# Optimization experiments

Measured on AMD Instinct MI355X. Metric: run time of the kernel, lower is better.

The kernel has to match this reference:

```python
import jax, jax.numpy as jnp
import numpy as np


def setup_inputs() -> dict:
    key = jax.random.key(0)
    k1, k2 = jax.random.split(key)
    num_experts, input_size, output_size = 8, 512, 512
    expert_size = 32768  # tokens per expert (equal load; total = 262144)
    total_tokens = num_experts * expert_size
    inputs = jax.random.normal(k1, (total_tokens, input_size), dtype=jnp.float32)
    # experts stored [num_experts, output_size, input_size], matching F.linear convention
    weight = jax.random.normal(k2, (num_experts, output_size, input_size), dtype=jnp.float32) * (1.0 / np.sqrt(input_size))
    return {"inputs": inputs, "weight": weight, "expert_size": expert_size}


def reference(inputs, weight, expert_size):
    # inputs: [T, in] sorted by expert, equal expert_size per expert.
    # Equivalent of: split by expert_size, F.linear(x_i, weight[i]), concat.
    num_experts = weight.shape[0]
    x = inputs.reshape(num_experts, expert_size, inputs.shape[-1])  # [E, t, in]
    out = jnp.einsum("eti,eoi->eto", x, weight)  # grouped GEMM, [E, t, out]
    return out.reshape(num_experts * expert_size, weight.shape[1])
```

## Files before the change

### kernel.cpp

```cpp
#include <hip/hip_runtime.h>
#include <hip/hip_bf16.h>

typedef __attribute__((ext_vector_type(4))) float f32x4;
typedef __attribute__((ext_vector_type(8))) short bf16x8;

#define BM 256
#define BN 256
#define BK 32
#define KDIM 512
#define NT (KDIM / BK)

__device__ __forceinline__ unsigned int bfpack(float a, float b) {
  __hip_bfloat162 h = __float22bfloat162_rn(float2{a, b});
  union { __hip_bfloat162 h2; unsigned int u; } c;
  c.h2 = h;
  return c.u;
}

__device__ __forceinline__ int swz(int row, int col) {
  return col ^ (((row >> 1) & 3) << 3);
}

__launch_bounds__(512, 2)
__global__ void moe_grouped_gemm(const float* __restrict__ A,
                                 const float* __restrict__ W,
                                 float* __restrict__ C) {
  __shared__ ushort As[2][BM][BK];
  __shared__ ushort Bs[2][BN][BK];

  const int tid  = threadIdx.x;
  const int lane = tid & 63;
  const int wid  = tid >> 6;
  const int wm   = wid >> 2;
  const int wn   = wid & 3;

  const int b  = blockIdx.x;
  const int e  = b & 7;
  const int t  = b >> 3;
  const int mt = t >> 1;
  const int nt = t & 1;

  const size_t mBase = (size_t)e * 32768 + (size_t)mt * BM;
  const int    nBase = nt * BN;

  const float* Ap = A + mBase * KDIM;
  const float* Wp = W + ((size_t)e * 512 + nBase) * KDIM;

  const int srow = tid >> 3;
  const int scol = (tid & 7) << 2;

  f32x4 acc[8][4];
  #pragma unroll
  for (int i = 0; i < 8; ++i)
    #pragma unroll
    for (int j = 0; j < 4; ++j)
      acc[i][j] = (f32x4){0.f, 0.f, 0.f, 0.f};

  float4 ra[4], rb[4];

  #pragma unroll
  for (int i = 0; i < 4; ++i) {
    const int row = srow + i * 64;
    ra[i] = *(const float4*)(Ap + row * KDIM + scol);
    rb[i] = *(const float4*)(Wp + row * KDIM + scol);
  }
  #pragma unroll
  for (int i = 0; i < 4; ++i) {
    const int row = srow + i * 64;
    const int sc  = swz(row, scol);
    uint2 pa, pb;
    pa.x = bfpack(ra[i].x, ra[i].y); pa.y = bfpack(ra[i].z, ra[i].w);
    pb.x = bfpack(rb[i].x, rb[i].y); pb.y = bfpack(rb[i].z, rb[i].w);
    *(uint2*)&As[0][row][sc] = pa;
    *(uint2*)&Bs[0][row][sc] = pb;
  }
  #pragma unroll
  for (int i = 0; i < 4; ++i) {
    const int row = srow + i * 64;
    ra[i] = *(const float4*)(Ap + row * KDIM + BK + scol);
    rb[i] = *(const float4*)(Wp + row * KDIM + BK + scol);
  }

  for (int kt = 0; kt < NT; ++kt) {
    __syncthreads();

    if (kt + 1 < NT) {
      const int nb = (kt + 1) & 1;
      #pragma unroll
      for (int i = 0; i < 4; ++i) {
        const int row = srow + i * 64;
        const int sc  = swz(row, scol);
        uint2 pa, pb;
        pa.x = bfpack(ra[i].x, ra[i].y); pa.y = bfpack(ra[i].z, ra[i].w);
        pb.x = bfpack(rb[i].x, rb[i].y); pb.y = bfpack(rb[i].z, rb[i].w);
        *(uint2*)&As[nb][row][sc] = pa;
        *(uint2*)&Bs[nb][row][sc] = pb;
      }
    }
    __builtin_amdgcn_sched_barrier(0);

    if (kt + 2 < NT) {
      const int k0 = (kt + 2) * BK;
      #pragma unroll
      for (int i = 0; i < 4; ++i) {
        const int row = srow + i * 64;
        ra[i] = *(const float4*)(Ap + row * KDIM + k0 + scol);
        rb[i] = *(const float4*)(Wp + row * KDIM + k0 + scol);
      }
    }
    __builtin_amdgcn_sched_barrier(0);

    {
      const int buf = kt & 1;
      const int kbase = (lane >> 4) << 3;
      bf16x8 bf[4];
      #pragma unroll
      for (int ni = 0; ni < 4; ++ni) {
        const int rrow = wn * 64 + ni * 16 + (lane & 15);
        bf[ni] = *(const bf16x8*)&Bs[buf][rrow][swz(rrow, kbase)];
      }
      #pragma unroll
      for (int mi = 0; mi < 8; ++mi) {
        const int arow = wm * 128 + mi * 16 + (lane & 15);
        const bf16x8 af = *(const bf16x8*)&As[buf][arow][swz(arow, kbase)];
        #pragma unroll
        for (int ni = 0; ni < 4; ++ni)
          acc[mi][ni] = __builtin_amdgcn_mfma_f32_16x16x32_bf16(af, bf[ni], acc[mi][ni], 0, 0, 0);
      }
    }
  }

  #pragma unroll
  for (int mi = 0; mi < 8; ++mi) {
    #pragma unroll
    for (int reg = 0; reg < 4; ++reg) {
      const int r = wm * 128 + mi * 16 + ((lane >> 4) << 2) + reg;
      float* rowp = C + (mBase + r) * 512 + nBase + wn * 64 + (lane & 15);
      #pragma unroll
      for (int ni = 0; ni < 4; ++ni)
        __builtin_nontemporal_store(acc[mi][ni][reg], rowp + ni * 16);
    }
  }
}

extern "C" void kernel_launch(void* const* d_in, const int* in_sizes, int n_in,
                              void* d_out, int out_size, void* d_ws, size_t ws_size,
                              hipStream_t stream) {
  const float* inputs = (const float*)d_in[0];
  const float* weight = (const float*)d_in[1];
  float* out = (float*)d_out;
  (void)d_ws; (void)ws_size; (void)in_sizes; (void)n_in;

  moe_grouped_gemm<<<2048, 512, 0, stream>>>(inputs, weight, out);
}
```

Measured before the change: 324.0 us.

## Stage fp32 tiles directly into LDS and convert to bf16 at fragment read

Replaces the register-staged global loads and bf16 packing before the LDS store with asynchronous global_load_lds transfers. Each k-tile is kept as fp32 in LDS with an XOR-swizzled layout, and values are converted to bf16 when MFMA fragments are read. The main loop is split into two MFMA half-phases with raw s_barrier and s_setprio to interleave waves. The cost is twice the LDS footprint, which likely drops occupancy below the two-block launch bound. It also duplicates the conversion work across the waves that share a fragment.

```diff
diff --git a/kernel.cpp b/kernel.cpp
--- a/kernel.cpp
+++ b/kernel.cpp
@@ -8,7 +8,7 @@
 #define BN 256
 #define BK 32
 #define KDIM 512
-#define NT (KDIM / BK)
+#define NT 16
 
 __device__ __forceinline__ unsigned int bfpack(float a, float b) {
   __hip_bfloat162 h = __float22bfloat162_rn(float2{a, b});
@@ -17,16 +17,35 @@
   return c.u;
 }
 
-__device__ __forceinline__ int swz(int row, int col) {
-  return col ^ (((row >> 1) & 3) << 3);
+typedef __attribute__((address_space(1))) const unsigned int gas_u32;
+typedef __attribute__((address_space(3))) unsigned int las_u32;
+
+__device__ __forceinline__ void gload16(const float* g, float* l) {
+  __builtin_amdgcn_global_load_lds((gas_u32*)(const void*)g, (las_u32*)(void*)l, 16, 0, 0);
+}
+
+__device__ __forceinline__ bf16x8 readfrag(const float* buf, int row, int fg) {
+  const int s = row & 7;
+  const f32x4 lo = *(const f32x4*)(buf + row * BK + ((fg ^ s) << 2));
+  const f32x4 hi = *(const f32x4*)(buf + row * BK + (((fg + 1) ^ s) << 2));
+  union { bf16x8 v; unsigned int u[4]; } r;
+  r.u[0] = bfpack(lo[0], lo[1]);
+  r.u[1] = bfpack(lo[2], lo[3]);
+  r.u[2] = bfpack(hi[0], hi[1]);
+  r.u[3] = bfpack(hi[2], hi[3]);
+  return r.v;
+}
+
+__device__ __forceinline__ void hw_barrier() {
+  asm volatile("s_barrier" ::: "memory");
 }
 
 __launch_bounds__(512, 2)
 __global__ void moe_grouped_gemm(const float* __restrict__ A,
                                  const float* __restrict__ W,
                                  float* __restrict__ C) {
-  __shared__ ushort As[2][BM][BK];
-  __shared__ ushort Bs[2][BN][BK];
+  __shared__ float As[2][BM * BK];
+  __shared__ float Bs[2][BN * BK];
 
   const int tid  = threadIdx.x;
   const int lane = tid & 63;
@@ -34,11 +53,11 @@
   const int wm   = wid >> 2;
   const int wn   = wid & 3;
 
-  const int b  = blockIdx.x;
-  const int e  = b & 7;
-  const int t  = b >> 3;
-  const int mt = t >> 1;
-  const int nt = t & 1;
+  const int bidx = blockIdx.x;
+  const int e  = bidx & 7;
+  const int tt = bidx >> 3;
+  const int mt = tt >> 1;
+  const int nt = tt & 1;
 
   const size_t mBase = (size_t)e * 32768 + (size_t)mt * BM;
   const int    nBase = nt * BN;
@@ -46,8 +65,22 @@
   const float* Ap = A + mBase * KDIM;
   const float* Wp = W + ((size_t)e * 512 + nBase) * KDIM;
 
-  const int srow = tid >> 3;
-  const int scol = (tid & 7) << 2;
+  const int srow = lane >> 3;
+  const int sg   = lane & 7;
+  const int fr = lane & 15;
+  const int fg = (lane >> 4) << 1;
+
+#define STAGE(tile, buf)                                                     \
+  {                                                                          \
+    const int tcol_ = (tile) * BK;                                           \
+    _Pragma("unroll")                                                        \
+    for (int i_ = 0; i_ < 4; ++i_) {                                         \
+      const int row_ = wid * 32 + i_ * 8 + srow;                             \
+      const int gc_  = tcol_ + ((sg ^ (row_ & 7)) << 2);                     \
+      gload16(Ap + (size_t)row_ * KDIM + gc_, &As[buf][(wid * 32 + i_ * 8) * BK]); \
+      gload16(Wp + (size_t)row_ * KDIM + gc_, &Bs[buf][(wid * 32 + i_ * 8) * BK]); \
+    }                                                                        \
+  }
 
   f32x4 acc[8][4];
   #pragma unroll
@@ -56,78 +89,52 @@
     for (int j = 0; j < 4; ++j)
       acc[i][j] = (f32x4){0.f, 0.f, 0.f, 0.f};
 
-  float4 ra[4], rb[4];
+  STAGE(0, 0);
+  STAGE(1, 1);
+  asm volatile("s_waitcnt vmcnt(8)" ::: "memory");
+  hw_barrier();
 
-  #pragma unroll
-  for (int i = 0; i < 4; ++i) {
-    const int row = srow + i * 64;
-    ra[i] = *(const float4*)(Ap + row * KDIM + scol);
-    rb[i] = *(const float4*)(Wp + row * KDIM + scol);
-  }
-  #pragma unroll
-  for (int i = 0; i < 4; ++i) {
-    const int row = srow + i * 64;
-    const int sc  = swz(row, scol);
-    uint2 pa, pb;
-    pa.x = bfpack(ra[i].x, ra[i].y); pa.y = bfpack(ra[i].z, ra[i].w);
-    pb.x = bfpack(rb[i].x, rb[i].y); pb.y = bfpack(rb[i].z, rb[i].w);
-    *(uint2*)&As[0][row][sc] = pa;
-    *(uint2*)&Bs[0][row][sc] = pb;
-  }
-  #pragma unroll
-  for (int i = 0; i < 4; ++i) {
-    const int row = srow + i * 64;
-    ra[i] = *(const float4*)(Ap + row * KDIM + BK + scol);
-    rb[i] = *(const float4*)(Wp + row * KDIM + BK + scol);
-  }
+  for (int t = 0; t < NT; ++t) {
+    const int bb = t & 1;
+    const float* Ab = &As[bb][0];
+    const float* Bb = &Bs[bb][0];
 
-  for (int kt = 0; kt < NT; ++kt) {
-    __syncthreads();
+    if (t >= 1 && t + 1 < NT) STAGE(t + 1, bb ^ 1);
 
-    if (kt + 1 < NT) {
-      const int nb = (kt + 1) & 1;
+    bf16x8 bfB[4];
+    #pragma unroll
+    for (int ni = 0; ni < 4; ++ni)
+      bfB[ni] = readfrag(Bb, wn * 64 + ni * 16 + fr, fg);
+    bf16x8 bfA[4];
+    #pragma unroll
+    for (int mi = 0; mi < 4; ++mi)
+      bfA[mi] = readfrag(Ab, wm * 128 + mi * 16 + fr, fg);
+
+    hw_barrier();
+    __builtin_amdgcn_s_setprio(1);
+    #pragma unroll
+    for (int mi = 0; mi < 4; ++mi)
       #pragma unroll
-      for (int i = 0; i < 4; ++i) {
-        const int row = srow + i * 64;
-        const int sc  = swz(row, scol);
-        uint2 pa, pb;
-        pa.x = bfpack(ra[i].x, ra[i].y); pa.y = bfpack(ra[i].z, ra[i].w);
-        pb.x = bfpack(rb[i].x, rb[i].y); pb.y = bfpack(rb[i].z, rb[i].w);
-        *(uint2*)&As[nb][row][sc] = pa;
-        *(uint2*)&Bs[nb][row][sc] = pb;
-      }
-    }
-    __builtin_amdgcn_sched_barrier(0);
+      for (int ni = 0; ni < 4; ++ni)
+        acc[mi][ni] = __builtin_amdgcn_mfma_f32_16x16x32_bf16(bfA[mi], bfB[ni], acc[mi][ni], 0, 0, 0);
+    __builtin_amdgcn_s_setprio(0);
+    hw_barrier();
 
-    if (kt + 2 < NT) {
-      const int k0 = (kt + 2) * BK;
+    #pragma unroll
+    for (int mi = 0; mi < 4; ++mi)
+      bfA[mi] = readfrag(Ab, wm * 128 + (mi + 4) * 16 + fr, fg);
+
+    hw_barrier();
+    __builtin_amdgcn_s_setprio(1);
+    #pragma unroll
+    for (int mi = 0; mi < 4; ++mi)
       #pragma unroll
-      for (int i = 0; i < 4; ++i) {
-        const int row = srow + i * 64;
-        ra[i] = *(const float4*)(Ap + row * KDIM + k0 + scol);
-        rb[i] = *(const float4*)(Wp + row * KDIM + k0 + scol);
-      }
-    }
-    __builtin_amdgcn_sched_barrier(0);
+      for (int ni = 0; ni < 4; ++ni)
+        acc[mi + 4][ni] = __builtin_amdgcn_mfma_f32_16x16x32_bf16(bfA[mi], bfB[ni], acc[mi + 4][ni], 0, 0, 0);
+    __builtin_amdgcn_s_setprio(0);
 
-    {
-      const int buf = kt & 1;
-      const int kbase = (lane >> 4) << 3;
-      bf16x8 bf[4];
-      #pragma unroll
-      for (int ni = 0; ni < 4; ++ni) {
-        const int rrow = wn * 64 + ni * 16 + (lane & 15);
-        bf[ni] = *(const bf16x8*)&Bs[buf][rrow][swz(rrow, kbase)];
-      }
-      #pragma unroll
-      for (int mi = 0; mi < 8; ++mi) {
-        const int arow = wm * 128 + mi * 16 + (lane & 15);
-        const bf16x8 af = *(const bf16x8*)&As[buf][arow][swz(arow, kbase)];
-        #pragma unroll
-        for (int ni = 0; ni < 4; ++ni)
-          acc[mi][ni] = __builtin_amdgcn_mfma_f32_16x16x32_bf16(af, bf[ni], acc[mi][ni], 0, 0, 0);
-      }
-    }
+    if (t + 1 < NT) asm volatile("s_waitcnt vmcnt(0)" ::: "memory");
+    hw_barrier();
   }
 
   #pragma unroll
@@ -141,6 +148,7 @@
         __builtin_nontemporal_store(acc[mi][ni][reg], rowp + ni * 16);
     }
   }
+#undef STAGE
 }
 
 extern "C" void kernel_launch(void* const* d_in, const int* in_sizes, int n_in,
```

Result: slower. 447.5 us (+38.1%).
